# Optimization experiments

Measured on AMD Instinct MI355X. Metric: run time of the kernel, lower is better.

The kernel has to match this reference:

```python
import jax, jax.numpy as jnp
import numpy as np

N_NODES = 50000
N_EDGES = 800000
IN_CH = 512
HIDDEN = 512


def setup_inputs() -> dict:
    key = jax.random.key(0)
    k1, k2, k3, k4 = jax.random.split(key, 4)
    x = jax.random.normal(k1, (N_NODES, IN_CH), dtype=jnp.float32)
    edge_index = jax.random.randint(k2, (2, N_EDGES), 0, N_NODES, dtype=jnp.int64)
    # Glorot-style scaling for weights
    W1 = jax.random.normal(k3, (IN_CH, HIDDEN), dtype=jnp.float32) / np.sqrt(IN_CH)
    b1 = jnp.zeros((HIDDEN,), dtype=jnp.float32)
    W2 = jax.random.normal(k4, (HIDDEN, 1), dtype=jnp.float32) / np.sqrt(HIDDEN)
    b2 = jnp.zeros((1,), dtype=jnp.float32)
    return {"x": x, "edge_index": edge_index, "W1": W1, "b1": b1, "W2": W2, "b2": b2}


def _gcn_conv(x, edge_index, W, b):
    """PyG GCNConv: add self-loops, symmetric D^{-1/2}(A+I)D^{-1/2} normalization."""
    N = x.shape[0]
    xw = x @ W                                   # [N, out]
    row, col = edge_index[0], edge_index[1]      # source -> target
    # degree on target nodes, +1 for the self-loop
    deg = jax.ops.segment_sum(jnp.ones_like(col, dtype=xw.dtype), col, num_segments=N) + 1.0
    dis = jax.lax.rsqrt(deg)                     # deg^{-1/2}, [N]
    norm = dis[row] * dis[col]                   # [E]
    agg = jax.ops.segment_sum(norm[:, None] * xw[row], col, num_segments=N)
    agg = agg + (dis * dis)[:, None] * xw        # self-loop contribution
    return agg + b


def reference(x, edge_index, W1, b1, W2, b2):
    h = jax.nn.relu(_gcn_conv(x, edge_index, W1, b1))
    # dropout in eval mode (training=False) -> identity
    out = _gcn_conv(h, edge_index, W2, b2)
    return out.squeeze(-1)                       # [N]
```

## Files before the change

### kernel.cpp

```cpp
#include <hip/hip_runtime.h>

#define IN_CH 512
#define SCAN_BLK 1024

typedef _Float16 f16x8 __attribute__((ext_vector_type(8)));
typedef float f32x4 __attribute__((ext_vector_type(4)));

__device__ __forceinline__ void gload_lds16(const void* g, void* l) {
    __builtin_amdgcn_global_load_lds(
        (const __attribute__((address_space(1))) unsigned int*)g,
        (__attribute__((address_space(3))) unsigned int*)l, 16, 0, 0);
}

__global__ __launch_bounds__(256) void k_merged1(const float* __restrict__ W1,
                                                 _Float16* __restrict__ W1t,
                                                 const int* __restrict__ col,
                                                 int* __restrict__ deg, int E, int N) {
    __shared__ float tile[32][33];
    if ((int)blockIdx.x >= 256) {
        int e = ((int)blockIdx.x - 256) * 256 + threadIdx.x;
        if (e < E) {
            int d = col[e];
            if ((unsigned)d < (unsigned)N) atomicAdd(&deg[d], 1);
        }
        return;
    }
    const int bk = (blockIdx.x & 15) * 32, bn = (blockIdx.x >> 4) * 32;
    const int tx = threadIdx.x & 31, ty = threadIdx.x >> 5;
#pragma unroll
    for (int p = 0; p < 4; ++p)
        tile[ty + p * 8][tx] = W1[(size_t)(bk + ty + p * 8) * 512 + bn + tx];
    __syncthreads();
#pragma unroll
    for (int p = 0; p < 4; ++p)
        W1t[(size_t)(bn + ty + p * 8) * 512 + bk + tx] = (_Float16)tile[tx][ty + p * 8];
}

__global__ __launch_bounds__(SCAN_BLK) void k_psum(const int* __restrict__ deg,
                                                   int* __restrict__ bsum, int N) {
    __shared__ int red[SCAN_BLK / 64];
    int i = blockIdx.x * SCAN_BLK + threadIdx.x;
    int v = (i < N) ? deg[i] : 0;
#pragma unroll
    for (int off = 32; off > 0; off >>= 1) v += __shfl_down(v, off);
    if ((threadIdx.x & 63) == 0) red[threadIdx.x >> 6] = v;
    __syncthreads();
    if (threadIdx.x == 0) {
        int s = 0;
#pragma unroll
        for (int u = 0; u < SCAN_BLK / 64; ++u) s += red[u];
        bsum[blockIdx.x] = s;
    }
}

__global__ __launch_bounds__(SCAN_BLK) void k_write(const int* __restrict__ deg,
                                                    const int* __restrict__ bsum,
                                                    int* __restrict__ rp,
                                                    float* __restrict__ dis,
                                                    int* __restrict__ cursor, int N) {
    __shared__ int sums[SCAN_BLK];
    __shared__ int boff_s, tot_s;
    int t = threadIdx.x;
    if (t < 64) {
        int v = (t < (int)gridDim.x) ? bsum[t] : 0;
        int pre = (t < (int)blockIdx.x) ? v : 0;
        int a = pre, b = v;
#pragma unroll
        for (int off = 32; off > 0; off >>= 1) {
            a += __shfl_down(a, off);
            b += __shfl_down(b, off);
        }
        if (t == 0) { boff_s = a; tot_s = b; }
    }
    int i = blockIdx.x * SCAN_BLK + t;
    int d = (i < N) ? deg[i] : 0;
    sums[t] = d;
    __syncthreads();
    for (int off = 1; off < SCAN_BLK; off <<= 1) {
        int u = (t >= off) ? sums[t - off] : 0;
        __syncthreads();
        sums[t] += u;
        __syncthreads();
    }
    if (i < N) {
        rp[i] = boff_s + sums[t] - d;
        dis[i] = rsqrtf((float)d + 1.0f);
        cursor[i] = 0;
    }
    if (blockIdx.x == gridDim.x - 1 && t == 0) rp[N] = tot_s;
}

__global__ __launch_bounds__(256) void k_merged2(const float* __restrict__ A,
                                                 const _Float16* __restrict__ Bt,
                                                 _Float16* __restrict__ C,
                                                 int Nrows, int nbm, int fillb,
                                                 const int* __restrict__ ei,
                                                 const int* __restrict__ rp,
                                                 int* __restrict__ cursor,
                                                 int* __restrict__ csrc,
                                                 int E, int N) {
    __shared__ __align__(16) _Float16 As[128 * 64];
    __shared__ __align__(16) _Float16 Bs[128 * 64];

    if ((int)blockIdx.x < fillb) {
        int e = (int)blockIdx.x * 256 + threadIdx.x;
        if (e < E) {
            int s = ei[e];
            int d = ei[E + e];
            if ((unsigned)s < (unsigned)N && (unsigned)d < (unsigned)N) {
                int pos = atomicAdd(&cursor[d], 1);
                csrc[rp[d] + pos] = s;
            }
        }
        return;
    }

    const int g = (int)blockIdx.x - fillb;
    const int nwg = nbm * 4;
    const int t = threadIdx.x;
    const int lane = t & 63, w = t >> 6;
    const int wm = w >> 1, wn = w & 1;

    const int q = nwg >> 3, r = nwg & 7;
    const int xcd = g & 7, within = g >> 3;
    const int wg = (xcd < r ? xcd * (q + 1) : r * (q + 1) + (xcd - r) * q) + within;
    const int bm = (wg >> 2) * 128, bn = (wg & 3) * 128;

    const int rr = lane & 15, kg = lane >> 4;
    const int lrow = lane >> 3, lcol = (lane & 7) * 8;
    const int arow = t >> 3, acol = (t & 7) * 8;

    f32x4 acc[4][4];
#pragma unroll
    for (int i = 0; i < 4; ++i)
#pragma unroll
        for (int j = 0; j < 4; ++j) acc[i][j] = (f32x4)0.0f;

    for (int k0 = 0; k0 < 512; k0 += 64) {
#pragma unroll
        for (int p = 0; p < 4; ++p) {
            const int row = p * 32 + w * 8 + lrow;
            gload_lds16(Bt + (size_t)(bn + row) * 512 + k0 + lcol,
                        Bs + (p * 32 + w * 8) * 64);
        }
#pragma unroll
        for (int p = 0; p < 4; ++p) {
            int grow = bm + p * 32 + arow;
            if (grow >= Nrows) grow = Nrows - 1;
            const float* gp = A + (size_t)grow * 512 + k0 + acol;
            float4 u0 = *(const float4*)gp;
            float4 u1 = *(const float4*)(gp + 4);
            f16x8 o;
            o[0] = (_Float16)u0.x; o[1] = (_Float16)u0.y;
            o[2] = (_Float16)u0.z; o[3] = (_Float16)u0.w;
            o[4] = (_Float16)u1.x; o[5] = (_Float16)u1.y;
            o[6] = (_Float16)u1.z; o[7] = (_Float16)u1.w;
            *(f16x8*)(As + ((p * 32 + arow) * 64 + acol)) = o;
        }
        __syncthreads();
#pragma unroll
        for (int kk = 0; kk < 2; ++kk) {
            f16x8 a[4], b[4];
#pragma unroll
            for (int i = 0; i < 4; ++i)
                a[i] = *(const f16x8*)(As + (wm * 64 + i * 16 + rr) * 64 + kk * 32 + kg * 8);
#pragma unroll
            for (int j = 0; j < 4; ++j)
                b[j] = *(const f16x8*)(Bs + (wn * 64 + j * 16 + rr) * 64 + kk * 32 + kg * 8);
#pragma unroll
            for (int i = 0; i < 4; ++i)
#pragma unroll
                for (int j = 0; j < 4; ++j)
                    acc[i][j] = __builtin_amdgcn_mfma_f32_16x16x32_f16(a[i], b[j], acc[i][j], 0, 0, 0);
        }
        __syncthreads();
    }

#pragma unroll
    for (int i = 0; i < 4; ++i)
#pragma unroll
        for (int j = 0; j < 4; ++j)
#pragma unroll
            for (int reg = 0; reg < 4; ++reg) {
                int m = bm + wm * 64 + i * 16 + kg * 4 + reg;
                int n = bn + wn * 64 + j * 16 + rr;
                C[(size_t)m * 512 + n] = (_Float16)acc[i][j][reg];
            }
}

__global__ __launch_bounds__(256) void k_agg(const _Float16* __restrict__ y,
                                             const float* __restrict__ dis,
                                             const int* __restrict__ rp,
                                             const int* __restrict__ csrc,
                                             const float* __restrict__ b1,
                                             const float* __restrict__ W2,
                                             float* __restrict__ z, int N) {
    const int n = blockIdx.x * 4 + (threadIdx.x >> 6);
    if (n >= N) return;
    const int l = threadIdx.x & 63;

    const float d1 = dis[n];
    f16x8 self = *(const f16x8*)(y + (size_t)n * 512 + l * 8);
    float acc[8];
#pragma unroll
    for (int c = 0; c < 8; ++c) acc[c] = d1 * (float)self[c];

    int j = rp[n], jend = rp[n + 1];
    for (; j + 8 <= jend; j += 8) {
        int s[8]; float wt[8]; f16x8 v[8];
#pragma unroll
        for (int u = 0; u < 8; ++u) s[u] = csrc[j + u];
#pragma unroll
        for (int u = 0; u < 8; ++u) wt[u] = dis[s[u]];
#pragma unroll
        for (int u = 0; u < 8; ++u)
            v[u] = *(const f16x8*)(y + (size_t)s[u] * 512 + l * 8);
#pragma unroll
        for (int u = 0; u < 8; ++u)
#pragma unroll
            for (int c = 0; c < 8; ++c) acc[c] += wt[u] * (float)v[u][c];
    }
    for (; j + 2 <= jend; j += 2) {
        int s0 = csrc[j], s1 = csrc[j + 1];
        float w0 = dis[s0], w1 = dis[s1];
        f16x8 v0 = *(const f16x8*)(y + (size_t)s0 * 512 + l * 8);
        f16x8 v1 = *(const f16x8*)(y + (size_t)s1 * 512 + l * 8);
#pragma unroll
        for (int c = 0; c < 8; ++c) acc[c] += w0 * (float)v0[c] + w1 * (float)v1[c];
    }
    if (j < jend) {
        int s0 = csrc[j];
        float w0 = dis[s0];
        f16x8 v0 = *(const f16x8*)(y + (size_t)s0 * 512 + l * 8);
#pragma unroll
        for (int c = 0; c < 8; ++c) acc[c] += w0 * (float)v0[c];
    }

    float4 bb0 = *(const float4*)(b1 + l * 8);
    float4 bb1 = *(const float4*)(b1 + l * 8 + 4);
    float4 w20 = *(const float4*)(W2 + l * 8);
    float4 w21 = *(const float4*)(W2 + l * 8 + 4);
    float bbv[8] = {bb0.x, bb0.y, bb0.z, bb0.w, bb1.x, bb1.y, bb1.z, bb1.w};
    float w2v[8] = {w20.x, w20.y, w20.z, w20.w, w21.x, w21.y, w21.z, w21.w};
    float p = 0.0f;
#pragma unroll
    for (int c = 0; c < 8; ++c) {
        float h = fmaxf(acc[c] * d1 + bbv[c], 0.0f);
        p += h * w2v[c];
    }
#pragma unroll
    for (int off = 32; off > 0; off >>= 1) p += __shfl_down(p, off);
    if (l == 0) z[n] = d1 * p;
}

__global__ void k_out(const float* __restrict__ z, const float* __restrict__ dis,
                      const int* __restrict__ rp, const int* __restrict__ csrc,
                      const float* __restrict__ b2, float* __restrict__ out, int N) {
    int n = blockIdx.x * blockDim.x + threadIdx.x;
    if (n >= N) return;
    float acc = z[n];
    int j = rp[n], jend = rp[n + 1];
    for (; j + 4 <= jend; j += 4) {
        float a0 = z[csrc[j]];
        float a1 = z[csrc[j + 1]];
        float a2 = z[csrc[j + 2]];
        float a3 = z[csrc[j + 3]];
        acc += (a0 + a1) + (a2 + a3);
    }
    for (; j < jend; ++j) acc += z[csrc[j]];
    out[n] = dis[n] * acc + b2[0];
}

extern "C" void kernel_launch(void* const* d_in, const int* in_sizes, int n_in,
                              void* d_out, int out_size, void* d_ws, size_t ws_size,
                              hipStream_t stream) {
    const float* x  = (const float*)d_in[0];
    const int*   ei = (const int*)d_in[1];
    const float* W1 = (const float*)d_in[2];
    const float* b1 = (const float*)d_in[3];
    const float* W2 = (const float*)d_in[4];
    const float* b2 = (const float*)d_in[5];
    float* out = (float*)d_out;

    const int N = in_sizes[0] / IN_CH;
    const int E = in_sizes[1] / 2;
    const int nbm = (N + 127) / 128;
    const int M2 = nbm * 128;
    const int NB = (N + SCAN_BLK - 1) / SCAN_BLK;
    const int DEGB  = (E + 255) / 256;
    const int FILLB = ((DEGB + 7) / 8) * 8;

    char* ws = (char*)d_ws;
    size_t off = 0;
    auto alloc = [&](size_t bytes) {
        char* p = ws + off;
        off += (bytes + 255) & ~(size_t)255;
        return p;
    };
    _Float16* y   = (_Float16*)alloc((size_t)M2 * 512 * sizeof(_Float16));
    _Float16* W1t = (_Float16*)alloc((size_t)512 * 512 * sizeof(_Float16));
    int*   deg    = (int*)alloc((size_t)N * sizeof(int));
    float* dis    = (float*)alloc((size_t)N * sizeof(float));
    int*   rp     = (int*)alloc((size_t)(N + 1) * sizeof(int));
    int*   cursor = (int*)alloc((size_t)N * sizeof(int));
    int*   csrc   = (int*)alloc((size_t)E * sizeof(int));
    float* z      = (float*)alloc((size_t)N * sizeof(float));
    int*   bsum   = (int*)alloc((size_t)64 * sizeof(int));

    hipMemsetAsync(deg, 0, (size_t)N * sizeof(int), stream);

    k_merged1<<<256 + DEGB, 256, 0, stream>>>(W1, W1t, ei + E, deg, E, N);
    k_psum<<<NB, SCAN_BLK, 0, stream>>>(deg, bsum, N);
    k_write<<<NB, SCAN_BLK, 0, stream>>>(deg, bsum, rp, dis, cursor, N);
    k_merged2<<<FILLB + nbm * 4, 256, 0, stream>>>(x, W1t, y, N, nbm, FILLB,
                                                   ei, rp, cursor, csrc, E, N);
    k_agg<<<(N + 3) / 4, 256, 0, stream>>>(y, dis, rp, csrc, b1, W2, z, N);
    k_out<<<(N + 255) / 256, 256, 0, stream>>>(z, dis, rp, csrc, b2, out, N);
}
```

Baseline: 263.7 us.

## Pre-convert x to fp16 and load both GEMM operands via swizzled LDS DMA

The fp32 to fp16 conversion of x moves into the first merged kernel, which writes a zero-padded half-precision copy. The GEMM can then load A tiles with global_load_lds directly, like B, and an XOR swizzle on the LDS column layout reduces bank conflicts on the MFMA fragment reads. The CSR-fill blocks are moved after the GEMM tiles in the grid. This adds an extra write and read of a 50 MB fp16 copy of x in exchange for simpler, asynchronous GEMM loads.

```diff
diff --git a/kernel.cpp b/kernel.cpp
--- a/kernel.cpp
+++ b/kernel.cpp
@@ -12,28 +12,50 @@
         (__attribute__((address_space(3))) unsigned int*)l, 16, 0, 0);
 }
 
-__global__ __launch_bounds__(256) void k_merged1(const float* __restrict__ W1,
+__global__ __launch_bounds__(256) void k_merged1(const int* __restrict__ col,
+                                                 int* __restrict__ deg, int E, int N,
+                                                 const float* __restrict__ W1,
                                                  _Float16* __restrict__ W1t,
-                                                 const int* __restrict__ col,
-                                                 int* __restrict__ deg, int E, int N) {
+                                                 const float* __restrict__ x,
+                                                 _Float16* __restrict__ xh,
+                                                 int degb, int total, int valid) {
     __shared__ float tile[32][33];
-    if ((int)blockIdx.x >= 256) {
-        int e = ((int)blockIdx.x - 256) * 256 + threadIdx.x;
+    const int bid = blockIdx.x;
+    if (bid < degb) {
+        int e = bid * 256 + threadIdx.x;
         if (e < E) {
             int d = col[e];
             if ((unsigned)d < (unsigned)N) atomicAdd(&deg[d], 1);
         }
         return;
     }
-    const int bk = (blockIdx.x & 15) * 32, bn = (blockIdx.x >> 4) * 32;
-    const int tx = threadIdx.x & 31, ty = threadIdx.x >> 5;
-#pragma unroll
-    for (int p = 0; p < 4; ++p)
-        tile[ty + p * 8][tx] = W1[(size_t)(bk + ty + p * 8) * 512 + bn + tx];
-    __syncthreads();
-#pragma unroll
-    for (int p = 0; p < 4; ++p)
-        W1t[(size_t)(bn + ty + p * 8) * 512 + bk + tx] = (_Float16)tile[tx][ty + p * 8];
+    if (bid < degb + 256) {
+        const int b = bid - degb;
+        const int bk = (b & 15) * 32, bn = (b >> 4) * 32;
+        const int tx = threadIdx.x & 31, ty = threadIdx.x >> 5;
+#pragma unroll
+        for (int p = 0; p < 4; ++p)
+            tile[ty + p * 8][tx] = W1[(size_t)(bk + ty + p * 8) * 512 + bn + tx];
+        __syncthreads();
+#pragma unroll
+        for (int p = 0; p < 4; ++p)
+            W1t[(size_t)(bn + ty + p * 8) * 512 + bk + tx] = (_Float16)tile[tx][ty + p * 8];
+        return;
+    }
+    int i = ((bid - degb - 256) * 256 + threadIdx.x) * 8;
+    if (i >= total) return;
+    f16x8 o;
+    if (i < valid) {
+        float4 v0 = *(const float4*)(x + i);
+        float4 v1 = *(const float4*)(x + i + 4);
+        o[0] = (_Float16)v0.x; o[1] = (_Float16)v0.y;
+        o[2] = (_Float16)v0.z; o[3] = (_Float16)v0.w;
+        o[4] = (_Float16)v1.x; o[5] = (_Float16)v1.y;
+        o[6] = (_Float16)v1.z; o[7] = (_Float16)v1.w;
+    } else {
+        o = (f16x8)0;
+    }
+    *(f16x8*)(xh + i) = o;
 }
 
 __global__ __launch_bounds__(SCAN_BLK) void k_psum(const int* __restrict__ deg,
@@ -90,10 +112,10 @@
     if (blockIdx.x == gridDim.x - 1 && t == 0) rp[N] = tot_s;
 }
 
-__global__ __launch_bounds__(256) void k_merged2(const float* __restrict__ A,
+__global__ __launch_bounds__(256) void k_merged2(const _Float16* __restrict__ A,
                                                  const _Float16* __restrict__ Bt,
                                                  _Float16* __restrict__ C,
-                                                 int Nrows, int nbm, int fillb,
+                                                 int nbm, int nwg,
                                                  const int* __restrict__ ei,
                                                  const int* __restrict__ rp,
                                                  int* __restrict__ cursor,
@@ -102,8 +124,8 @@
     __shared__ __align__(16) _Float16 As[128 * 64];
     __shared__ __align__(16) _Float16 Bs[128 * 64];
 
-    if ((int)blockIdx.x < fillb) {
-        int e = (int)blockIdx.x * 256 + threadIdx.x;
+    if ((int)blockIdx.x >= nwg) {
+        int e = ((int)blockIdx.x - nwg) * 256 + threadIdx.x;
         if (e < E) {
             int s = ei[e];
             int d = ei[E + e];
@@ -115,8 +137,7 @@
         return;
     }
 
-    const int g = (int)blockIdx.x - fillb;
-    const int nwg = nbm * 4;
+    const int g = (int)blockIdx.x;
     const int t = threadIdx.x;
     const int lane = t & 63, w = t >> 6;
     const int wm = w >> 1, wn = w & 1;
@@ -127,8 +148,9 @@
     const int bm = (wg >> 2) * 128, bn = (wg & 3) * 128;
 
     const int rr = lane & 15, kg = lane >> 4;
-    const int lrow = lane >> 3, lcol = (lane & 7) * 8;
-    const int arow = t >> 3, acol = (t & 7) * 8;
+    const int lrow = lane >> 3;
+    const int scol = ((lane & 7) ^ lrow) * 8;
+    const int rsw = rr & 7;
 
     f32x4 acc[4][4];
 #pragma unroll
@@ -140,22 +162,9 @@
 #pragma unroll
         for (int p = 0; p < 4; ++p) {
             const int row = p * 32 + w * 8 + lrow;
-            gload_lds16(Bt + (size_t)(bn + row) * 512 + k0 + lcol,
-                        Bs + (p * 32 + w * 8) * 64);
-        }
-#pragma unroll
-        for (int p = 0; p < 4; ++p) {
-            int grow = bm + p * 32 + arow;
-            if (grow >= Nrows) grow = Nrows - 1;
-            const float* gp = A + (size_t)grow * 512 + k0 + acol;
-            float4 u0 = *(const float4*)gp;
-            float4 u1 = *(const float4*)(gp + 4);
-            f16x8 o;
-            o[0] = (_Float16)u0.x; o[1] = (_Float16)u0.y;
-            o[2] = (_Float16)u0.z; o[3] = (_Float16)u0.w;
-            o[4] = (_Float16)u1.x; o[5] = (_Float16)u1.y;
-            o[6] = (_Float16)u1.z; o[7] = (_Float16)u1.w;
-            *(f16x8*)(As + ((p * 32 + arow) * 64 + acol)) = o;
+            const int ldsbase = (p * 32 + w * 8) * 64;
+            gload_lds16(A + (size_t)(bm + row) * 512 + k0 + scol, As + ldsbase);
+            gload_lds16(Bt + (size_t)(bn + row) * 512 + k0 + scol, Bs + ldsbase);
         }
         __syncthreads();
 #pragma unroll
@@ -163,10 +172,12 @@
             f16x8 a[4], b[4];
 #pragma unroll
             for (int i = 0; i < 4; ++i)
-                a[i] = *(const f16x8*)(As + (wm * 64 + i * 16 + rr) * 64 + kk * 32 + kg * 8);
+                a[i] = *(const f16x8*)(As + (wm * 64 + i * 16 + rr) * 64 +
+                                       (((kk << 2) + kg) ^ rsw) * 8);
 #pragma unroll
             for (int j = 0; j < 4; ++j)
-                b[j] = *(const f16x8*)(Bs + (wn * 64 + j * 16 + rr) * 64 + kk * 32 + kg * 8);
+                b[j] = *(const f16x8*)(Bs + (wn * 64 + j * 16 + rr) * 64 +
+                                       (((kk << 2) + kg) ^ rsw) * 8);
 #pragma unroll
             for (int i = 0; i < 4; ++i)
 #pragma unroll
@@ -287,8 +298,9 @@
     const int nbm = (N + 127) / 128;
     const int M2 = nbm * 128;
     const int NB = (N + SCAN_BLK - 1) / SCAN_BLK;
-    const int DEGB  = (E + 255) / 256;
-    const int FILLB = ((DEGB + 7) / 8) * 8;
+    const int DEGB = (E + 255) / 256;
+    const int CVTB = (M2 * 512) / 2048;
+    const int nwg  = nbm * 4;
 
     char* ws = (char*)d_ws;
     size_t off = 0;
@@ -297,6 +309,7 @@
         off += (bytes + 255) & ~(size_t)255;
         return p;
     };
+    _Float16* xh  = (_Float16*)alloc((size_t)M2 * 512 * sizeof(_Float16));
     _Float16* y   = (_Float16*)alloc((size_t)M2 * 512 * sizeof(_Float16));
     _Float16* W1t = (_Float16*)alloc((size_t)512 * 512 * sizeof(_Float16));
     int*   deg    = (int*)alloc((size_t)N * sizeof(int));
@@ -309,11 +322,13 @@
 
     hipMemsetAsync(deg, 0, (size_t)N * sizeof(int), stream);
 
-    k_merged1<<<256 + DEGB, 256, 0, stream>>>(W1, W1t, ei + E, deg, E, N);
+    k_merged1<<<DEGB + 256 + CVTB, 256, 0, stream>>>(ei + E, deg, E, N,
+                                                     W1, W1t, x, xh,
+                                                     DEGB, M2 * 512, N * 512);
     k_psum<<<NB, SCAN_BLK, 0, stream>>>(deg, bsum, N);
     k_write<<<NB, SCAN_BLK, 0, stream>>>(deg, bsum, rp, dis, cursor, N);
-    k_merged2<<<FILLB + nbm * 4, 256, 0, stream>>>(x, W1t, y, N, nbm, FILLB,
-                                                   ei, rp, cursor, csrc, E, N);
+    k_merged2<<<nwg + DEGB, 256, 0, stream>>>(xh, W1t, y, nbm, nwg,
+                                              ei, rp, cursor, csrc, E, N);
     k_agg<<<(N + 3) / 4, 256, 0, stream>>>(y, dis, rp, csrc, b1, W2, z, N);
     k_out<<<(N + 255) / 256, 256, 0, stream>>>(z, dis, rp, csrc, b2, out, N);
 }
```

Result: slower. 271.5 us (+3.0%).

## XOR-swizzle GEMM LDS tiles and launch CSR fill blocks after GEMM blocks

Applied to the files above, without the earlier changes.

Applies an XOR swizzle to the 16-byte chunk column in both the A and B LDS tiles of the fused GEMM, for both the stores and the MFMA fragment reads. The aim is to remove LDS bank conflicts when each wave reads 16-row fragments with a 128-byte row stride. It also reorders the merged launch so GEMM workgroups take the low block indices and the CSR fill blocks follow them, which changes scheduling priority and the XCD mapping. The swizzle has to match exactly between the global-to-LDS loads and the reads, or the results will be wrong.

```diff
diff --git a/kernel.cpp b/kernel.cpp
--- a/kernel.cpp
+++ b/kernel.cpp
@@ -93,7 +93,7 @@
 __global__ __launch_bounds__(256) void k_merged2(const float* __restrict__ A,
                                                  const _Float16* __restrict__ Bt,
                                                  _Float16* __restrict__ C,
-                                                 int Nrows, int nbm, int fillb,
+                                                 int Nrows, int nbm, int nwg,
                                                  const int* __restrict__ ei,
                                                  const int* __restrict__ rp,
                                                  int* __restrict__ cursor,
@@ -102,8 +102,8 @@
     __shared__ __align__(16) _Float16 As[128 * 64];
     __shared__ __align__(16) _Float16 Bs[128 * 64];
 
-    if ((int)blockIdx.x < fillb) {
-        int e = (int)blockIdx.x * 256 + threadIdx.x;
+    if ((int)blockIdx.x >= nwg) {
+        int e = ((int)blockIdx.x - nwg) * 256 + threadIdx.x;
         if (e < E) {
             int s = ei[e];
             int d = ei[E + e];
@@ -115,8 +115,7 @@
         return;
     }
 
-    const int g = (int)blockIdx.x - fillb;
-    const int nwg = nbm * 4;
+    const int g = (int)blockIdx.x;
     const int t = threadIdx.x;
     const int lane = t & 63, w = t >> 6;
     const int wm = w >> 1, wn = w & 1;
@@ -127,8 +126,12 @@
     const int bm = (wg >> 2) * 128, bn = (wg & 3) * 128;
 
     const int rr = lane & 15, kg = lane >> 4;
-    const int lrow = lane >> 3, lcol = (lane & 7) * 8;
-    const int arow = t >> 3, acol = (t & 7) * 8;
+    const int lrow = lane >> 3;
+    const int scol = ((lane & 7) ^ lrow) * 8;
+    const int rsw = rr & 7;
+    const int arow = t >> 3;
+    const int achk = t & 7;
+    const int agcol = (achk ^ (arow & 7)) * 8;
 
     f32x4 acc[4][4];
 #pragma unroll
@@ -140,14 +143,14 @@
 #pragma unroll
         for (int p = 0; p < 4; ++p) {
             const int row = p * 32 + w * 8 + lrow;
-            gload_lds16(Bt + (size_t)(bn + row) * 512 + k0 + lcol,
+            gload_lds16(Bt + (size_t)(bn + row) * 512 + k0 + scol,
                         Bs + (p * 32 + w * 8) * 64);
         }
 #pragma unroll
         for (int p = 0; p < 4; ++p) {
             int grow = bm + p * 32 + arow;
             if (grow >= Nrows) grow = Nrows - 1;
-            const float* gp = A + (size_t)grow * 512 + k0 + acol;
+            const float* gp = A + (size_t)grow * 512 + k0 + agcol;
             float4 u0 = *(const float4*)gp;
             float4 u1 = *(const float4*)(gp + 4);
             f16x8 o;
@@ -155,7 +158,7 @@
             o[2] = (_Float16)u0.z; o[3] = (_Float16)u0.w;
             o[4] = (_Float16)u1.x; o[5] = (_Float16)u1.y;
             o[6] = (_Float16)u1.z; o[7] = (_Float16)u1.w;
-            *(f16x8*)(As + ((p * 32 + arow) * 64 + acol)) = o;
+            *(f16x8*)(As + (p * 32 + arow) * 64 + achk * 8) = o;
         }
         __syncthreads();
 #pragma unroll
@@ -163,10 +166,12 @@
             f16x8 a[4], b[4];
 #pragma unroll
             for (int i = 0; i < 4; ++i)
-                a[i] = *(const f16x8*)(As + (wm * 64 + i * 16 + rr) * 64 + kk * 32 + kg * 8);
+                a[i] = *(const f16x8*)(As + (wm * 64 + i * 16 + rr) * 64 +
+                                       (((kk << 2) + kg) ^ rsw) * 8);
 #pragma unroll
             for (int j = 0; j < 4; ++j)
-                b[j] = *(const f16x8*)(Bs + (wn * 64 + j * 16 + rr) * 64 + kk * 32 + kg * 8);
+                b[j] = *(const f16x8*)(Bs + (wn * 64 + j * 16 + rr) * 64 +
+                                       (((kk << 2) + kg) ^ rsw) * 8);
 #pragma unroll
             for (int i = 0; i < 4; ++i)
 #pragma unroll
@@ -287,8 +292,8 @@
     const int nbm = (N + 127) / 128;
     const int M2 = nbm * 128;
     const int NB = (N + SCAN_BLK - 1) / SCAN_BLK;
-    const int DEGB  = (E + 255) / 256;
-    const int FILLB = ((DEGB + 7) / 8) * 8;
+    const int DEGB = (E + 255) / 256;
+    const int nwg  = nbm * 4;
 
     char* ws = (char*)d_ws;
     size_t off = 0;
@@ -312,8 +317,8 @@
     k_merged1<<<256 + DEGB, 256, 0, stream>>>(W1, W1t, ei + E, deg, E, N);
     k_psum<<<NB, SCAN_BLK, 0, stream>>>(deg, bsum, N);
     k_write<<<NB, SCAN_BLK, 0, stream>>>(deg, bsum, rp, dis, cursor, N);
-    k_merged2<<<FILLB + nbm * 4, 256, 0, stream>>>(x, W1t, y, N, nbm, FILLB,
-                                                   ei, rp, cursor, csrc, E, N);
+    k_merged2<<<nwg + DEGB, 256, 0, stream>>>(x, W1t, y, N, nbm, nwg,
+                                              ei, rp, cursor, csrc, E, N);
     k_agg<<<(N + 3) / 4, 256, 0, stream>>>(y, dis, rp, csrc, b1, W2, z, N);
     k_out<<<(N + 255) / 256, 256, 0, stream>>>(z, dis, rp, csrc, b2, out, N);
 }
```

After: 251.0 us. 4.8% less time.
